# Performance work log

Measured on AMD Instinct MI355X. Metric: run time of the kernel, lower is better.

## Reference

```python
import jax, jax.numpy as jnp
import numpy as np

M, N, D, P = 16, 4096, 128, 8192
H = N // D


def setup_inputs() -> dict:
    key = jax.random.key(0)
    ks = jax.random.split(key, 6)
    return {
        "X": jax.random.normal(ks[0], (M, N), dtype=jnp.float32),
        "W_q": jax.random.normal(ks[1], (N, N), dtype=jnp.float32) / np.sqrt(N),
        "W_k": jax.random.normal(ks[2], (N, N), dtype=jnp.float32) / np.sqrt(N),
        "W_v": jax.random.normal(ks[3], (N, N), dtype=jnp.float32) / np.sqrt(N),
        "cache_K": jax.random.normal(ks[4], (H, P, D), dtype=jnp.float32),
        "cache_V": jax.random.normal(ks[5], (H, P, D), dtype=jnp.float32),
    }


def _rms(x):
    # unaffine RMS norm over last dim, no eps (matches torch source)
    return x * jax.lax.rsqrt(jnp.mean(jnp.square(x), axis=-1, keepdims=True))


def reference(X, W_q, W_k, W_v, cache_K, cache_V):
    m, n = X.shape
    h, p, d = cache_K.shape
    # QKV projections -> [H, M, D]
    q = (X @ W_q).reshape(m, h, d).swapaxes(0, 1)
    k = (X @ W_k).reshape(m, h, d).swapaxes(0, 1)
    v = (X @ W_v).reshape(m, h, d).swapaxes(0, 1)
    q_norm = _rms(q)
    k_norm = _rms(k)
    # prepend KV cache: [H, P+M, D]
    k_cache = jnp.concatenate([cache_K[:, :p, :], k_norm], axis=1)
    v_cache = jnp.concatenate([cache_V[:, :p, :], v], axis=1)
    # attention WITHOUT 1/sqrt(D) scaling (matches torch source)
    scores = jnp.einsum("hmd,hpd->hmp", q_norm, k_cache)
    weights = jax.nn.softmax(scores, axis=-1)
    out = jnp.einsum("hmp,hpd->hmd", weights, v_cache)  # [H, M, D]
    return out.swapaxes(0, 1).reshape(m, n)
```

## Files before the change

kernel.cpp:

```cpp
#include <hip/hip_runtime.h>
#include <math.h>

#define M_ 16
#define N_ 4096
#define D_ 128
#define P_ 8192
#define H_ 32

#define NIC 32
#define ICH (N_/NIC)
#define NCB 16

#define CHUNK 128
#define NCH (P_/CHUNK)
#define NCH1 (NCH+1)

#define QKV_SZ    (3*H_*M_*D_)
#define PART_OFF  (QKV_SZ)
#define OPART_OFF (QKV_SZ)
#define OPART_SZ  (H_*NCH1*M_*D_)
#define ML_OFF    (OPART_OFF + OPART_SZ)

__global__ __launch_bounds__(256) void k_proj(const float* __restrict__ X,
                                              const float* __restrict__ Wq,
                                              const float* __restrict__ Wk,
                                              const float* __restrict__ Wv,
                                              float* __restrict__ part) {
  const int mat = blockIdx.z;
  const float* __restrict__ W = (mat == 0) ? Wq : ((mat == 1) ? Wk : Wv);
  const int cb = blockIdx.x, ic = blockIdx.y;
  const int t = threadIdx.x;
  const int j0 = cb * 256 + t;
  const int i0 = ic * ICH;

  __shared__ __align__(16) float XT[ICH][20];

  {
    const int i_l = t & 127, mh = t >> 7;
#pragma unroll
    for (int r = 0; r < 8; ++r)
      XT[i_l][mh * 8 + r] = X[(size_t)(mh * 8 + r) * N_ + i0 + i_l];
  }
  __syncthreads();

  float acc[16];
#pragma unroll
  for (int m = 0; m < 16; ++m) acc[m] = 0.f;

#pragma unroll 8
  for (int i = 0; i < ICH; ++i) {
    const float wv = __builtin_nontemporal_load(W + (size_t)(i0 + i) * N_ + j0);
    float xr[16];
    {
      float4 xv;
      xv = *reinterpret_cast<const float4*>(&XT[i][0]);
      xr[0] = xv.x; xr[1] = xv.y; xr[2] = xv.z; xr[3] = xv.w;
      xv = *reinterpret_cast<const float4*>(&XT[i][4]);
      xr[4] = xv.x; xr[5] = xv.y; xr[6] = xv.z; xr[7] = xv.w;
      xv = *reinterpret_cast<const float4*>(&XT[i][8]);
      xr[8] = xv.x; xr[9] = xv.y; xr[10] = xv.z; xr[11] = xv.w;
      xv = *reinterpret_cast<const float4*>(&XT[i][12]);
      xr[12] = xv.x; xr[13] = xv.y; xr[14] = xv.z; xr[15] = xv.w;
    }
#pragma unroll
    for (int m = 0; m < 16; ++m) acc[m] = fmaf(xr[m], wv, acc[m]);
  }

#pragma unroll
  for (int m = 0; m < 16; ++m)
    __builtin_nontemporal_store(acc[m], part + (size_t)((mat * NIC + ic) * M_ + m) * N_ + j0);
}

__global__ __launch_bounds__(256) void k_reduce(const float* __restrict__ part,
                                                float* __restrict__ qkv) {
  const int mat = blockIdx.z, m = blockIdx.y, nc = blockIdx.x;
  const int t = threadIdx.x;
  const int n = nc * 256 + t;

  float s = 0.f;
#pragma unroll
  for (int ic = 0; ic < NIC; ++ic)
    s += __builtin_nontemporal_load(part + (size_t)((mat * NIC + ic) * M_ + m) * N_ + n);

  float ss = s * s;
#pragma unroll
  for (int off = 1; off < 64; off <<= 1) ss += __shfl_xor(ss, off);
  __shared__ float wsum[4];
  const int wave = t >> 6, lane = t & 63;
  if (lane == 0) wsum[wave] = ss;
  __syncthreads();
  const int half = t >> 7;
  const float tot = wsum[half * 2] + wsum[half * 2 + 1];
  const float scale = (mat < 2) ? rsqrtf(tot * (1.0f / 128.0f)) : 1.0f;

  const int h = n >> 7, d = n & 127;
  qkv[(size_t)((mat * H_ + h) * M_ + m) * D_ + d] = s * scale;
}

__device__ __forceinline__ float fold8(float a[8], int dq) {
#pragma unroll
  for (int i = 0; i < 4; ++i) {
    const float send = (dq & 4) ? a[i] : a[i + 4];
    const float recv = __shfl_xor(send, 4);
    a[i] = ((dq & 4) ? a[i + 4] : a[i]) + recv;
  }
#pragma unroll
  for (int i = 0; i < 2; ++i) {
    const float send = (dq & 2) ? a[i] : a[i + 2];
    const float recv = __shfl_xor(send, 2);
    a[i] = ((dq & 2) ? a[i + 2] : a[i]) + recv;
  }
  {
    const float send = (dq & 1) ? a[0] : a[1];
    const float recv = __shfl_xor(send, 1);
    a[0] = ((dq & 1) ? a[1] : a[0]) + recv;
  }
  return a[0];
}

__global__ __launch_bounds__(512, 2) void k_attn(const float* __restrict__ cacheK,
                                                 const float* __restrict__ cacheV,
                                                 const float* __restrict__ qkv,
                                                 float* __restrict__ opart,
                                                 float* __restrict__ ml) {
  const int c = blockIdx.x, h = blockIdx.y;
  const int t = threadIdx.x;
  const int wave = t >> 6, lane = t & 63;
  const int valid = (c < NCH) ? CHUNK : M_;
  const float* __restrict__ Ksrc = (c < NCH)
      ? (cacheK + ((size_t)h * P_ + (size_t)c * CHUNK) * D_)
      : (qkv + (size_t)((1 * H_ + h) * M_) * D_);
  const float* __restrict__ Vsrc = (c < NCH)
      ? (cacheV + ((size_t)h * P_ + (size_t)c * CHUNK) * D_)
      : (qkv + (size_t)((2 * H_ + h) * M_) * D_);

  __shared__ __align__(16) float smem[8192];
  __shared__ __align__(16) float mlx[8][8][2];

  float* qs = smem;
  float* wxp = smem + 2048 + wave * 128;

  {
    const float4* src = reinterpret_cast<const float4*>(qkv + (size_t)(h * M_) * D_);
    reinterpret_cast<float4*>(qs)[t] = src[t];
  }
  __syncthreads();

  const int pg = lane >> 3, dq = lane & 7;
  const int dl = lane * 2;
  const int rg = wave >> 1, mbase = (wave & 1) * 8;
  const int rbase = rg * 32;
  int rc = valid - rbase; rc = (rc < 0) ? 0 : ((rc > 32) ? 32 : rc);
  const int nb = rc >> 4;

  float mrun = -3.0e38f, lrun = 0.f;
  float2 o[8];
#pragma unroll
  for (int mi = 0; mi < 8; ++mi) o[mi] = make_float2(0.f, 0.f);

  float4 kk[8];
  if (nb > 0) {
    const float* ka = Ksrc + (size_t)(rbase + pg) * D_ + dq * 4;
    kk[0] = *reinterpret_cast<const float4*>(ka);
    kk[1] = *reinterpret_cast<const float4*>(ka + 32);
    kk[2] = *reinterpret_cast<const float4*>(ka + 64);
    kk[3] = *reinterpret_cast<const float4*>(ka + 96);
    const float* kb = Ksrc + (size_t)(rbase + 8 + pg) * D_ + dq * 4;
    kk[4] = *reinterpret_cast<const float4*>(kb);
    kk[5] = *reinterpret_cast<const float4*>(kb + 32);
    kk[6] = *reinterpret_cast<const float4*>(kb + 64);
    kk[7] = *reinterpret_cast<const float4*>(kb + 96);
  }

#pragma unroll 1
  for (int b = 0; b < nb; ++b) {
    const int r0 = rbase + b * 16;

    float aA[8], aB[8];
#pragma unroll
    for (int mi = 0; mi < 8; ++mi) {
      const float* qrow = qs + (mbase + mi) * D_ + dq * 4;
      const float4 q0 = *reinterpret_cast<const float4*>(qrow);
      const float4 q1 = *reinterpret_cast<const float4*>(qrow + 32);
      const float4 q2 = *reinterpret_cast<const float4*>(qrow + 64);
      const float4 q3 = *reinterpret_cast<const float4*>(qrow + 96);
      float sa, sb;
      sa = q0.x * kk[0].x;
      sa = fmaf(q0.y, kk[0].y, sa); sa = fmaf(q0.z, kk[0].z, sa); sa = fmaf(q0.w, kk[0].w, sa);
      sa = fmaf(q1.x, kk[1].x, sa); sa = fmaf(q1.y, kk[1].y, sa);
      sa = fmaf(q1.z, kk[1].z, sa); sa = fmaf(q1.w, kk[1].w, sa);
      sa = fmaf(q2.x, kk[2].x, sa); sa = fmaf(q2.y, kk[2].y, sa);
      sa = fmaf(q2.z, kk[2].z, sa); sa = fmaf(q2.w, kk[2].w, sa);
      sa = fmaf(q3.x, kk[3].x, sa); sa = fmaf(q3.y, kk[3].y, sa);
      sa = fmaf(q3.z, kk[3].z, sa); sa = fmaf(q3.w, kk[3].w, sa);
      sb = q0.x * kk[4].x;
      sb = fmaf(q0.y, kk[4].y, sb); sb = fmaf(q0.z, kk[4].z, sb); sb = fmaf(q0.w, kk[4].w, sb);
      sb = fmaf(q1.x, kk[5].x, sb); sb = fmaf(q1.y, kk[5].y, sb);
      sb = fmaf(q1.z, kk[5].z, sb); sb = fmaf(q1.w, kk[5].w, sb);
      sb = fmaf(q2.x, kk[6].x, sb); sb = fmaf(q2.y, kk[6].y, sb);
      sb = fmaf(q2.z, kk[6].z, sb); sb = fmaf(q2.w, kk[6].w, sb);
      sb = fmaf(q3.x, kk[7].x, sb); sb = fmaf(q3.y, kk[7].y, sb);
      sb = fmaf(q3.z, kk[7].z, sb); sb = fmaf(q3.w, kk[7].w, sb);
      aA[mi] = sa; aB[mi] = sb;
      __builtin_amdgcn_sched_barrier(0);
    }

    float2 vvA[8], vvB[8];
#pragma unroll
    for (int j = 0; j < 8; ++j)
      vvA[j] = *reinterpret_cast<const float2*>(Vsrc + (size_t)(r0 + j) * D_ + dl);
#pragma unroll
    for (int j = 0; j < 8; ++j)
      vvB[j] = *reinterpret_cast<const float2*>(Vsrc + (size_t)(r0 + 8 + j) * D_ + dl);

    {
      int rn = r0 + 16 + pg;
      rn = (rn < valid) ? rn : (valid - 1);
      const float* ka = Ksrc + (size_t)rn * D_ + dq * 4;
      kk[0] = *reinterpret_cast<const float4*>(ka);
      kk[1] = *reinterpret_cast<const float4*>(ka + 32);
      kk[2] = *reinterpret_cast<const float4*>(ka + 64);
      kk[3] = *reinterpret_cast<const float4*>(ka + 96);
      int rn2 = r0 + 24 + pg;
      rn2 = (rn2 < valid) ? rn2 : (valid - 1);
      const float* kb = Ksrc + (size_t)rn2 * D_ + dq * 4;
      kk[4] = *reinterpret_cast<const float4*>(kb);
      kk[5] = *reinterpret_cast<const float4*>(kb + 32);
      kk[6] = *reinterpret_cast<const float4*>(kb + 64);
      kk[7] = *reinterpret_cast<const float4*>(kb + 96);
    }

    const float sA = fold8(aA, dq);
    const float sB = fold8(aB, dq);
    float tmax = fmaxf(sA, sB);
    tmax = fmaxf(tmax, __shfl_xor(tmax, 8));
    tmax = fmaxf(tmax, __shfl_xor(tmax, 16));
    tmax = fmaxf(tmax, __shfl_xor(tmax, 32));
    const float mnew = fmaxf(mrun, tmax);
    const float fc = __expf(mrun - mnew);
    mrun = mnew;
    const float wA = __expf(sA - mnew);
    const float wB = __expf(sB - mnew);
    float rs = wA + wB;
    rs += __shfl_xor(rs, 8); rs += __shfl_xor(rs, 16); rs += __shfl_xor(rs, 32);
    lrun = lrun * fc + rs;

    wxp[pg * 8 + dq] = wA;
    wxp[(8 + pg) * 8 + dq] = wB;

#pragma unroll
    for (int mi = 0; mi < 8; ++mi) {
      const float fcm = __shfl(fc, (lane & 56) | mi);
      o[mi].x *= fcm; o[mi].y *= fcm;
    }

#pragma unroll
    for (int j = 0; j < 8; ++j) {
      const float4 w0 = *reinterpret_cast<const float4*>(&wxp[j * 8]);
      const float4 w1 = *reinterpret_cast<const float4*>(&wxp[j * 8 + 4]);
      const float2 v = vvA[j];
#define PVM(i, wc) o[i].x = fmaf(wc, v.x, o[i].x); o[i].y = fmaf(wc, v.y, o[i].y);
      PVM(0, w0.x) PVM(1, w0.y) PVM(2, w0.z) PVM(3, w0.w)
      PVM(4, w1.x) PVM(5, w1.y) PVM(6, w1.z) PVM(7, w1.w)
#undef PVM
      if (j & 1) __builtin_amdgcn_sched_barrier(0);
    }
#pragma unroll
    for (int j = 0; j < 8; ++j) {
      const float4 w0 = *reinterpret_cast<const float4*>(&wxp[(8 + j) * 8]);
      const float4 w1 = *reinterpret_cast<const float4*>(&wxp[(8 + j) * 8 + 4]);
      const float2 v = vvB[j];
#define PVM(i, wc) o[i].x = fmaf(wc, v.x, o[i].x); o[i].y = fmaf(wc, v.y, o[i].y);
      PVM(0, w0.x) PVM(1, w0.y) PVM(2, w0.z) PVM(3, w0.w)
      PVM(4, w1.x) PVM(5, w1.y) PVM(6, w1.z) PVM(7, w1.w)
#undef PVM
      if (j & 1) __builtin_amdgcn_sched_barrier(0);
    }
  }

  __syncthreads();
  float* obuf = smem;
#pragma unroll
  for (int mi = 0; mi < 8; ++mi)
    *reinterpret_cast<float2*>(&obuf[wave * 1024 + mi * 128 + dl]) = o[mi];
  if (lane < 8) { mlx[wave][lane][0] = mrun; mlx[wave][lane][1] = lrun; }
  __syncthreads();

  {
    const int mm = t >> 5, seg = t & 31;
    const int w0i = mm >> 3, mi = mm & 7;
    float mv[4], lv[4];
#pragma unroll
    for (int r = 0; r < 4; ++r) { mv[r] = mlx[r * 2 + w0i][mi][0]; lv[r] = mlx[r * 2 + w0i][mi][1]; }
    const float mstar = fmaxf(fmaxf(mv[0], mv[1]), fmaxf(mv[2], mv[3]));
    float ew[4];
    float T = 0.f;
#pragma unroll
    for (int r = 0; r < 4; ++r) { ew[r] = __expf(mv[r] - mstar); T = fmaf(lv[r], ew[r], T); }
    float4 acc = make_float4(0.f, 0.f, 0.f, 0.f);
#pragma unroll
    for (int r = 0; r < 4; ++r) {
      const float4 v = *reinterpret_cast<const float4*>(&obuf[(r * 2 + w0i) * 1024 + mi * 128 + seg * 4]);
      acc.x = fmaf(ew[r], v.x, acc.x); acc.y = fmaf(ew[r], v.y, acc.y);
      acc.z = fmaf(ew[r], v.z, acc.z); acc.w = fmaf(ew[r], v.w, acc.w);
    }
    const size_t base = (size_t)((h * NCH1 + c) * M_ + mm) * D_;
    *reinterpret_cast<float4*>(opart + base + seg * 4) = acc;
    if (seg == 0) {
      ml[((size_t)(h * NCH1 + c) * M_ + mm) * 2 + 0] = mstar;
      ml[((size_t)(h * NCH1 + c) * M_ + mm) * 2 + 1] = T;
    }
  }
}

__global__ __launch_bounds__(128) void k_comb(const float* __restrict__ opart,
                                              const float* __restrict__ ml,
                                              float* __restrict__ out) {
  const int m = blockIdx.x, h = blockIdx.y, t = threadIdx.x;
  __shared__ float Ms[NCH1], Ls[NCH1];
  if (t < NCH1) {
    Ms[t] = ml[((size_t)(h * NCH1 + t) * M_ + m) * 2 + 0];
    Ls[t] = ml[((size_t)(h * NCH1 + t) * M_ + m) * 2 + 1];
  }
  __syncthreads();
  float gM = -3.0e38f;
#pragma unroll
  for (int c2 = 0; c2 < NCH1; ++c2) gM = fmaxf(gM, Ms[c2]);

  const float* __restrict__ ob = opart + (size_t)h * NCH1 * M_ * D_ + (size_t)m * D_ + t;
  float T = 0.f, o0 = 0.f, o1 = 0.f, o2 = 0.f, o3 = 0.f;
#pragma unroll 4
  for (int c2 = 0; c2 < NCH1 - 1; c2 += 4) {
    const float f0 = __expf(Ms[c2 + 0] - gM);
    const float f1 = __expf(Ms[c2 + 1] - gM);
    const float f2 = __expf(Ms[c2 + 2] - gM);
    const float f3 = __expf(Ms[c2 + 3] - gM);
    T = fmaf(Ls[c2 + 0], f0, T); T = fmaf(Ls[c2 + 1], f1, T);
    T = fmaf(Ls[c2 + 2], f2, T); T = fmaf(Ls[c2 + 3], f3, T);
    o0 = fmaf(ob[(size_t)(c2 + 0) * M_ * D_], f0, o0);
    o1 = fmaf(ob[(size_t)(c2 + 1) * M_ * D_], f1, o1);
    o2 = fmaf(ob[(size_t)(c2 + 2) * M_ * D_], f2, o2);
    o3 = fmaf(ob[(size_t)(c2 + 3) * M_ * D_], f3, o3);
  }
  {
    const int c2 = NCH1 - 1;
    const float f = __expf(Ms[c2] - gM);
    T = fmaf(Ls[c2], f, T);
    o0 = fmaf(ob[(size_t)c2 * M_ * D_], f, o0);
  }
  out[(size_t)m * N_ + h * D_ + t] = (o0 + o1 + o2 + o3) / T;
}

extern "C" void kernel_launch(void* const* d_in, const int* in_sizes, int n_in,
                              void* d_out, int out_size, void* d_ws, size_t ws_size,
                              hipStream_t stream) {
  const float* X  = (const float*)d_in[0];
  const float* Wq = (const float*)d_in[1];
  const float* Wk = (const float*)d_in[2];
  const float* Wv = (const float*)d_in[3];
  const float* cK = (const float*)d_in[4];
  const float* cV = (const float*)d_in[5];
  float* ws    = (float*)d_ws;
  float* qkv   = ws;
  float* part  = ws + PART_OFF;
  float* opart = ws + OPART_OFF;
  float* mlbuf = ws + ML_OFF;
  float* out   = (float*)d_out;

  hipLaunchKernelGGL(k_proj,   dim3(NCB, NIC, 3), dim3(256), 0, stream, X, Wq, Wk, Wv, part);
  hipLaunchKernelGGL(k_reduce, dim3(16, M_, 3),   dim3(256), 0, stream, part, qkv);
  hipLaunchKernelGGL(k_attn,   dim3(NCH1, H_),    dim3(512), 0, stream, cK, cV, qkv, opart, mlbuf);
  hipLaunchKernelGGL(k_comb,   dim3(M_, H_),      dim3(128), 0, stream, opart, mlbuf, out);
}
```

Before: 144.6 us.

## Halve attention chunk size, use 256-thread blocks, store partial outputs as bf16

Attention now splits the KV cache into chunks of 64 rows instead of 128 and runs 256-thread blocks, which doubles the number of blocks and shortens each block's work. Partial output vectors are written in bf16 to halve their write and read traffic in the combine kernel, and the V loads are issued before the QK dot products to hide their latency. In exchange, the combine step has twice as many partials to merge, and storing intermediates in bf16 costs some precision.

```diff
diff --git a/kernel.cpp b/kernel.cpp
--- a/kernel.cpp
+++ b/kernel.cpp
@@ -1,4 +1,5 @@
 #include <hip/hip_runtime.h>
+#include <hip/hip_bf16.h>
 #include <math.h>
 
 #define M_ 16
@@ -11,15 +12,15 @@
 #define ICH (N_/NIC)
 #define NCB 16
 
-#define CHUNK 128
+#define CHUNK 64
 #define NCH (P_/CHUNK)
 #define NCH1 (NCH+1)
 
-#define QKV_SZ    (3*H_*M_*D_)
-#define PART_OFF  (QKV_SZ)
-#define OPART_OFF (QKV_SZ)
-#define OPART_SZ  (H_*NCH1*M_*D_)
-#define ML_OFF    (OPART_OFF + OPART_SZ)
+#define QKV_SZ       (3*H_*M_*D_)
+#define PART_OFF     (QKV_SZ)
+#define OPART_OFF    (QKV_SZ)
+#define OPART_HALFSZ ((H_*NCH1*M_*D_)/2)
+#define ML_OFF       (OPART_OFF + OPART_HALFSZ)
 
 __global__ __launch_bounds__(256) void k_proj(const float* __restrict__ X,
                                               const float* __restrict__ Wq,
@@ -118,10 +119,17 @@
   return a[0];
 }
 
-__global__ __launch_bounds__(512, 2) void k_attn(const float* __restrict__ cacheK,
+__device__ __forceinline__ unsigned pk2(float a, float b) {
+  __hip_bfloat16 ha = __float2bfloat16(a), hb = __float2bfloat16(b);
+  const unsigned short ua = *reinterpret_cast<unsigned short*>(&ha);
+  const unsigned short ub = *reinterpret_cast<unsigned short*>(&hb);
+  return (unsigned)ua | ((unsigned)ub << 16);
+}
+
+__global__ __launch_bounds__(256, 2) void k_attn(const float* __restrict__ cacheK,
                                                  const float* __restrict__ cacheV,
                                                  const float* __restrict__ qkv,
-                                                 float* __restrict__ opart,
+                                                 __hip_bfloat16* __restrict__ opart,
                                                  float* __restrict__ ml) {
   const int c = blockIdx.x, h = blockIdx.y;
   const int t = threadIdx.x;
@@ -134,15 +142,17 @@
       ? (cacheV + ((size_t)h * P_ + (size_t)c * CHUNK) * D_)
       : (qkv + (size_t)((2 * H_ + h) * M_) * D_);
 
-  __shared__ __align__(16) float smem[8192];
-  __shared__ __align__(16) float mlx[8][8][2];
+  __shared__ __align__(16) float smem[4096];
+  __shared__ __align__(16) float wx[4 * 128];
+  __shared__ __align__(16) float mlx[4][8][2];
 
   float* qs = smem;
-  float* wxp = smem + 2048 + wave * 128;
+  float* wxp = wx + wave * 128;
 
   {
     const float4* src = reinterpret_cast<const float4*>(qkv + (size_t)(h * M_) * D_);
     reinterpret_cast<float4*>(qs)[t] = src[t];
+    reinterpret_cast<float4*>(qs)[t + 256] = src[t + 256];
   }
   __syncthreads();
 
@@ -175,6 +185,14 @@
 #pragma unroll 1
   for (int b = 0; b < nb; ++b) {
     const int r0 = rbase + b * 16;
+
+    float2 vvA[8], vvB[8];
+#pragma unroll
+    for (int j = 0; j < 8; ++j)
+      vvA[j] = *reinterpret_cast<const float2*>(Vsrc + (size_t)(r0 + j) * D_ + dl);
+#pragma unroll
+    for (int j = 0; j < 8; ++j)
+      vvB[j] = *reinterpret_cast<const float2*>(Vsrc + (size_t)(r0 + 8 + j) * D_ + dl);
 
     float aA[8], aB[8];
 #pragma unroll
@@ -205,14 +223,6 @@
       __builtin_amdgcn_sched_barrier(0);
     }
 
-    float2 vvA[8], vvB[8];
-#pragma unroll
-    for (int j = 0; j < 8; ++j)
-      vvA[j] = *reinterpret_cast<const float2*>(Vsrc + (size_t)(r0 + j) * D_ + dl);
-#pragma unroll
-    for (int j = 0; j < 8; ++j)
-      vvB[j] = *reinterpret_cast<const float2*>(Vsrc + (size_t)(r0 + 8 + j) * D_ + dl);
-
     {
       int rn = r0 + 16 + pg;
       rn = (rn < valid) ? rn : (valid - 1);
@@ -287,25 +297,24 @@
   __syncthreads();
 
   {
-    const int mm = t >> 5, seg = t & 31;
-    const int w0i = mm >> 3, mi = mm & 7;
-    float mv[4], lv[4];
-#pragma unroll
-    for (int r = 0; r < 4; ++r) { mv[r] = mlx[r * 2 + w0i][mi][0]; lv[r] = mlx[r * 2 + w0i][mi][1]; }
-    const float mstar = fmaxf(fmaxf(mv[0], mv[1]), fmaxf(mv[2], mv[3]));
-    float ew[4];
-    float T = 0.f;
-#pragma unroll
-    for (int r = 0; r < 4; ++r) { ew[r] = __expf(mv[r] - mstar); T = fmaf(lv[r], ew[r], T); }
-    float4 acc = make_float4(0.f, 0.f, 0.f, 0.f);
-#pragma unroll
-    for (int r = 0; r < 4; ++r) {
-      const float4 v = *reinterpret_cast<const float4*>(&obuf[(r * 2 + w0i) * 1024 + mi * 128 + seg * 4]);
-      acc.x = fmaf(ew[r], v.x, acc.x); acc.y = fmaf(ew[r], v.y, acc.y);
-      acc.z = fmaf(ew[r], v.z, acc.z); acc.w = fmaf(ew[r], v.w, acc.w);
-    }
-    const size_t base = (size_t)((h * NCH1 + c) * M_ + mm) * D_;
-    *reinterpret_cast<float4*>(opart + base + seg * 4) = acc;
+    const int mm = t >> 4, seg = t & 15;
+    const int mh = mm >> 3, mi = mm & 7;
+    const float m0v = mlx[mh][mi][0], m1v = mlx[2 + mh][mi][0];
+    const float mstar = fmaxf(m0v, m1v);
+    const float e0 = __expf(m0v - mstar), e1 = __expf(m1v - mstar);
+    const float T = mlx[mh][mi][1] * e0 + mlx[2 + mh][mi][1] * e1;
+    const float4 a0 = *reinterpret_cast<const float4*>(&obuf[mh * 1024 + mi * 128 + seg * 8]);
+    const float4 a1 = *reinterpret_cast<const float4*>(&obuf[mh * 1024 + mi * 128 + seg * 8 + 4]);
+    const float4 b0 = *reinterpret_cast<const float4*>(&obuf[(2 + mh) * 1024 + mi * 128 + seg * 8]);
+    const float4 b1 = *reinterpret_cast<const float4*>(&obuf[(2 + mh) * 1024 + mi * 128 + seg * 8 + 4]);
+    float r0 = e0 * a0.x + e1 * b0.x, r1 = e0 * a0.y + e1 * b0.y;
+    float r2 = e0 * a0.z + e1 * b0.z, r3 = e0 * a0.w + e1 * b0.w;
+    float r4 = e0 * a1.x + e1 * b1.x, r5 = e0 * a1.y + e1 * b1.y;
+    float r6 = e0 * a1.z + e1 * b1.z, r7 = e0 * a1.w + e1 * b1.w;
+    uint4 pk;
+    pk.x = pk2(r0, r1); pk.y = pk2(r2, r3); pk.z = pk2(r4, r5); pk.w = pk2(r6, r7);
+    const size_t base = ((size_t)(h * NCH1 + c) * M_ + mm) * D_ + seg * 8;
+    *reinterpret_cast<uint4*>(opart + base) = pk;
     if (seg == 0) {
       ml[((size_t)(h * NCH1 + c) * M_ + mm) * 2 + 0] = mstar;
       ml[((size_t)(h * NCH1 + c) * M_ + mm) * 2 + 1] = T;
@@ -313,21 +322,22 @@
   }
 }
 
-__global__ __launch_bounds__(128) void k_comb(const float* __restrict__ opart,
+__global__ __launch_bounds__(128) void k_comb(const __hip_bfloat16* __restrict__ opart,
                                               const float* __restrict__ ml,
                                               float* __restrict__ out) {
   const int m = blockIdx.x, h = blockIdx.y, t = threadIdx.x;
   __shared__ float Ms[NCH1], Ls[NCH1];
-  if (t < NCH1) {
-    Ms[t] = ml[((size_t)(h * NCH1 + t) * M_ + m) * 2 + 0];
-    Ls[t] = ml[((size_t)(h * NCH1 + t) * M_ + m) * 2 + 1];
+  for (int i = t; i < NCH1; i += 128) {
+    Ms[i] = ml[((size_t)(h * NCH1 + i) * M_ + m) * 2 + 0];
+    Ls[i] = ml[((size_t)(h * NCH1 + i) * M_ + m) * 2 + 1];
   }
   __syncthreads();
   float gM = -3.0e38f;
-#pragma unroll
+#pragma unroll 8
   for (int c2 = 0; c2 < NCH1; ++c2) gM = fmaxf(gM, Ms[c2]);
 
-  const float* __restrict__ ob = opart + (size_t)h * NCH1 * M_ * D_ + (size_t)m * D_ + t;
+  const __hip_bfloat16* __restrict__ ob =
+      opart + (size_t)h * NCH1 * M_ * D_ + (size_t)m * D_ + t;
   float T = 0.f, o0 = 0.f, o1 = 0.f, o2 = 0.f, o3 = 0.f;
 #pragma unroll 4
   for (int c2 = 0; c2 < NCH1 - 1; c2 += 4) {
@@ -337,16 +347,16 @@
     const float f3 = __expf(Ms[c2 + 3] - gM);
     T = fmaf(Ls[c2 + 0], f0, T); T = fmaf(Ls[c2 + 1], f1, T);
     T = fmaf(Ls[c2 + 2], f2, T); T = fmaf(Ls[c2 + 3], f3, T);
-    o0 = fmaf(ob[(size_t)(c2 + 0) * M_ * D_], f0, o0);
-    o1 = fmaf(ob[(size_t)(c2 + 1) * M_ * D_], f1, o1);
-    o2 = fmaf(ob[(size_t)(c2 + 2) * M_ * D_], f2, o2);
-    o3 = fmaf(ob[(size_t)(c2 + 3) * M_ * D_], f3, o3);
+    o0 = fmaf(__bfloat162float(ob[(size_t)(c2 + 0) * M_ * D_]), f0, o0);
+    o1 = fmaf(__bfloat162float(ob[(size_t)(c2 + 1) * M_ * D_]), f1, o1);
+    o2 = fmaf(__bfloat162float(ob[(size_t)(c2 + 2) * M_ * D_]), f2, o2);
+    o3 = fmaf(__bfloat162float(ob[(size_t)(c2 + 3) * M_ * D_]), f3, o3);
   }
   {
     const int c2 = NCH1 - 1;
     const float f = __expf(Ms[c2] - gM);
     T = fmaf(Ls[c2], f, T);
-    o0 = fmaf(ob[(size_t)c2 * M_ * D_], f, o0);
+    o0 = fmaf(__bfloat162float(ob[(size_t)c2 * M_ * D_]), f, o0);
   }
   out[(size_t)m * N_ + h * D_ + t] = (o0 + o1 + o2 + o3) / T;
 }
@@ -363,12 +373,12 @@
   float* ws    = (float*)d_ws;
   float* qkv   = ws;
   float* part  = ws + PART_OFF;
-  float* opart = ws + OPART_OFF;
+  __hip_bfloat16* opart = (__hip_bfloat16*)(ws + OPART_OFF);
   float* mlbuf = ws + ML_OFF;
   float* out   = (float*)d_out;
 
   hipLaunchKernelGGL(k_proj,   dim3(NCB, NIC, 3), dim3(256), 0, stream, X, Wq, Wk, Wv, part);
   hipLaunchKernelGGL(k_reduce, dim3(16, M_, 3),   dim3(256), 0, stream, part, qkv);
-  hipLaunchKernelGGL(k_attn,   dim3(NCH1, H_),    dim3(512), 0, stream, cK, cV, qkv, opart, mlbuf);
+  hipLaunchKernelGGL(k_attn,   dim3(NCH1, H_),    dim3(256), 0, stream, cK, cV, qkv, opart, mlbuf);
   hipLaunchKernelGGL(k_comb,   dim3(M_, H_),      dim3(128), 0, stream, opart, mlbuf, out);
 }
```

Measured after the change: 133.0 us. 1.09x faster.
